# Performance work log

Measured on AMD Instinct MI355X. Metric: run time of the kernel, lower is better.

The kernel has to match this reference:

```python
import jax, jax.numpy as jnp
import numpy as np

N = 100000
E = 1600000
D = 256

def setup_inputs() -> dict:
    key = jax.random.key(0)
    k1, k2, k3 = jax.random.split(key, 3)
    nodes = jax.random.normal(k1, (N, D), dtype=jnp.float32)
    edge_index = jax.random.randint(k2, (2, E), 0, N, dtype=jnp.int64)
    W = jax.random.normal(k3, (D, D), dtype=jnp.float32) * 0.05  # GCN lin weight [out,in]
    b = jnp.zeros((D,), dtype=jnp.float32)
    gamma = jnp.ones((D,), dtype=jnp.float32)
    beta = jnp.zeros((D,), dtype=jnp.float32)
    return {"nodes": nodes, "edge_index": edge_index, "W": W, "b": b,
            "gamma": gamma, "beta": beta}

def reference(nodes, edge_index, W, b, gamma, beta):
    n = nodes.shape[0]
    loop = jnp.arange(n, dtype=edge_index.dtype)
    src = jnp.concatenate([edge_index[0], loop])  # add self-loops (PyG default)
    dst = jnp.concatenate([edge_index[1], loop])
    # linear transform
    x = nodes @ W.T  # [N, D]
    # symmetric normalization: deg from target index, weight 1 per edge
    deg = jnp.zeros((n,), dtype=x.dtype).at[dst].add(1.0)
    dinv = jnp.where(deg > 0, jax.lax.rsqrt(deg), 0.0)
    norm = dinv[src] * dinv[dst]  # [E+N]
    msg = x[src] * norm[:, None]
    out = jax.ops.segment_sum(msg, dst, num_segments=n) + b  # [N, D]
    # LayerNorm over feature dim
    mu = jnp.mean(out, axis=-1, keepdims=True)
    var = jnp.mean(jnp.square(out - mu), axis=-1, keepdims=True)
    out = (out - mu) * jax.lax.rsqrt(var + 1e-5) * gamma + beta
    # ReLU; dropout is identity in eval mode
    return jax.nn.relu(out)
```

## Files before the change

### kernel.cpp

```cpp
#include <hip/hip_runtime.h>
#include <hip/hip_bf16.h>

#define NN 100000
#define EE 1600000
#define DD 256
#define CAP 48
#define NPART 391
#define ABLK 800
#define ACHUNK 2000

typedef __bf16 bf16x8 __attribute__((ext_vector_type(8)));
typedef float f32x4 __attribute__((ext_vector_type(4)));
typedef float f32x2 __attribute__((ext_vector_type(2)));

__device__ __forceinline__ unsigned short f2bf(float f) {
    unsigned u = __builtin_bit_cast(unsigned, f);
    u += 0x7fffu + ((u >> 16) & 1u);
    return (unsigned short)(u >> 16);
}
__device__ __forceinline__ float bf2f(unsigned short h) {
    unsigned u = ((unsigned)h) << 16;
    return __builtin_bit_cast(float, u);
}

__global__ __launch_bounds__(256) void k_partA(const void* __restrict__ eptr,
        unsigned int* __restrict__ gseg2, int* __restrict__ cnts, int* __restrict__ pref) {
    __shared__ int lcnt[NPART];
    __shared__ int lcnt2[NPART];
    __shared__ int lpref[NPART];
    __shared__ int sA[512], sB[512];
    __shared__ __align__(16) unsigned int stash[ACHUNK];
    __shared__ unsigned short stashp[ACHUNK];
    __shared__ __align__(16) unsigned int sorted[ACHUNK];
    __shared__ int lflag;
    const int b = blockIdx.x, tid = threadIdx.x;
    if (tid == 0) lflag = 0;
    for (int i = tid; i < NPART; i += 256) { lcnt[i] = 0; lcnt2[i] = 0; }
    __syncthreads();
    if (tid < 64) {
        const unsigned long long w = ((const unsigned long long*)eptr)[tid];
        if (w > 0xFFFFFFFFULL) lflag = 1;
    }
    __syncthreads();
    const int is32 = lflag;
    const int e0 = b * ACHUNK;
    for (int e = e0 + tid; e < e0 + ACHUNK; e += 256) {
        int ss, dd;
        if (is32) { const int* p = (const int*)eptr; ss = p[e]; dd = p[EE + e]; }
        else { const long long* p = (const long long*)eptr; ss = (int)p[e]; dd = (int)p[EE + e]; }
        const int li = e - e0;
        stash[li]  = ((unsigned)ss << 8) | (unsigned)(dd & 255);
        stashp[li] = (unsigned short)(dd >> 8);
        atomicAdd(&lcnt[dd >> 8], 1);
    }
    __syncthreads();
    sA[tid]       = (tid < NPART) ? lcnt[tid] : 0;
    sA[tid + 256] = (tid + 256 < NPART) ? lcnt[tid + 256] : 0;
    __syncthreads();
    int* s = sA; int* d2 = sB;
    for (int off = 1; off < 512; off <<= 1) {
        d2[tid]       = s[tid]       + (tid >= off ? s[tid - off] : 0);
        d2[tid + 256] = s[tid + 256] + (tid + 256 >= off ? s[tid + 256 - off] : 0);
        __syncthreads();
        int* t = s; s = d2; d2 = t;
    }
    for (int i = tid; i < NPART; i += 256) {
        lpref[i] = (i == 0) ? 0 : s[i - 1];
        cnts[(size_t)i * ABLK + b] = lcnt[i];
        pref[(size_t)i * ABLK + b] = (i == 0) ? 0 : s[i - 1];
    }
    __syncthreads();
    for (int li = tid; li < ACHUNK; li += 256) {
        const unsigned int w = stash[li];
        const int pp = stashp[li];
        const int slot = atomicAdd(&lcnt2[pp], 1);
        sorted[lpref[pp] + slot] = w;
    }
    __syncthreads();
    for (int li4 = tid; li4 < ACHUNK / 4; li4 += 256)
        *(uint4*)(gseg2 + (size_t)b * ACHUNK + (size_t)li4 * 4) = *(const uint4*)&sorted[li4 * 4];
}

__global__ __launch_bounds__(256) void k_partB(const unsigned int* __restrict__ gseg2,
        const int* __restrict__ cnts, const int* __restrict__ pref,
        int* __restrict__ bucket, int* __restrict__ cnt) {
    __shared__ int lc[256];
    __shared__ __align__(16) int lb[256 * CAP];
    const int p = blockIdx.x, tid = threadIdx.x;
    const int node0 = p * 256 + tid;
    lc[tid] = 1;
    lb[tid * CAP] = node0;
    __syncthreads();
    for (int bb = tid; bb < ABLK; bb += 256) {
        const int c = cnts[(size_t)p * ABLK + bb];
        const unsigned int* seg = gseg2 + (size_t)bb * ACHUNK + pref[(size_t)p * ABLK + bb];
        for (int i = 0; i < c; ++i) {
            const unsigned int en = seg[i];
            const int d = en & 255;
            const int slot = atomicAdd(&lc[d], 1);
            if (slot < CAP) lb[d * CAP + slot] = (int)(en >> 8);
        }
    }
    __syncthreads();
    const size_t base = (size_t)p * 256 * CAP;
    #pragma unroll
    for (int it = 0; it < CAP / 4; ++it) {
        const int idx4 = it * 256 + tid;
        const int node = p * 256 + idx4 / (CAP / 4);
        if (node < NN)
            *(uint4*)(bucket + base + (size_t)idx4 * 4) = *(const uint4*)&lb[idx4 * 4];
    }
    if (node0 < NN) cnt[node0] = lc[tid];
}

__global__ void k_detect(const unsigned long long* __restrict__ e64, int* __restrict__ flag) {
    if (threadIdx.x == 0 && blockIdx.x == 0) {
        int is32 = 0;
        for (int i = 0; i < 64; ++i)
            if (e64[i] > 0xFFFFFFFFULL) is32 = 1;
        *flag = is32;
    }
}
__global__ __launch_bounds__(256) void k_init(int* __restrict__ cnt, int* __restrict__ bucket) {
    int v = blockIdx.x * 256 + threadIdx.x;
    if (v < NN) { cnt[v] = 1; bucket[(size_t)v * CAP] = v; }
}
__global__ __launch_bounds__(256) void k_count_scatter(const void* __restrict__ eptr,
        const int* __restrict__ flag, int* __restrict__ cnt, int* __restrict__ bucket) {
    int e = blockIdx.x * 256 + threadIdx.x;
    if (e >= EE) return;
    int s, d;
    if (*flag) { const int* p = (const int*)eptr; s = p[e]; d = p[EE + e]; }
    else { const long long* p = (const long long*)eptr; s = (int)p[e]; d = (int)p[EE + e]; }
    int slot = atomicAdd(&cnt[d], 1);
    if (slot < CAP) bucket[(size_t)d * CAP + slot] = s;
}

__global__ __launch_bounds__(256) void k_wconv(const float* __restrict__ W,
        unsigned short* __restrict__ wf) {
    const int s = blockIdx.x * 256 + threadIdx.x;
    const int lane = s & 63;
    const int ks = (s >> 6) & 7;
    const int g  = (s >> 9) & 3;
    const int wv = s >> 11;
    const int feat = wv * 64 + g * 16 + (lane & 15);
    const int k0 = ks * 32 + (lane >> 4) * 8;
    const float* wp = W + (size_t)feat * 256 + k0;
    unsigned short o[8];
    #pragma unroll
    for (int j = 0; j < 8; ++j) o[j] = f2bf(wp[j]);
    uint4 pk;
    pk.x = o[0] | ((unsigned)o[1] << 16); pk.y = o[2] | ((unsigned)o[3] << 16);
    pk.z = o[4] | ((unsigned)o[5] << 16); pk.w = o[6] | ((unsigned)o[7] << 16);
    *(uint4*)(wf + (size_t)s * 8) = pk;
}

__global__ __launch_bounds__(256) void k_gemm(const float* __restrict__ nodes,
        const unsigned short* __restrict__ wf, const int* __restrict__ cnt,
        unsigned short* __restrict__ y) {
    __shared__ __align__(16) unsigned short xlds[64][264];
    const int tid = threadIdx.x, lane = tid & 63, wv = tid >> 6;
    const int q = lane >> 4, n0 = lane & 15;

    bf16x8 afrag[8][4];
    #pragma unroll
    for (int g = 0; g < 4; ++g)
        #pragma unroll
        for (int ks = 0; ks < 8; ++ks)
            afrag[ks][g] = *(const bf16x8*)(wf + ((((size_t)wv * 4 + g) * 8 + ks) * 64 + lane) * 8);

    const int row0 = blockIdx.x * 64;
    #pragma unroll
    for (int rr = 0; rr < 16; ++rr) {
        const int idx = rr * 256 + tid;
        const int r = idx >> 6, c4 = idx & 63;
        const int grow = min(row0 + r, NN - 1);
        const float4 v = *(const float4*)(nodes + (size_t)grow * 256 + c4 * 4);
        uint2 pk;
        pk.x = (unsigned)f2bf(v.x) | ((unsigned)f2bf(v.y) << 16);
        pk.y = (unsigned)f2bf(v.z) | ((unsigned)f2bf(v.w) << 16);
        *(uint2*)&xlds[r][c4 * 4] = pk;
    }
    __syncthreads();

    #pragma unroll
    for (int sub = 0; sub < 4; ++sub) {
        f32x4 acc[4] = {{0,0,0,0},{0,0,0,0},{0,0,0,0},{0,0,0,0}};
        #pragma unroll
        for (int ks = 0; ks < 8; ++ks) {
            const bf16x8 xf = *(const bf16x8*)&xlds[sub * 16 + n0][ks * 32 + q * 8];
            #pragma unroll
            for (int g = 0; g < 4; ++g)
                acc[g] = __builtin_amdgcn_mfma_f32_16x16x32_bf16(afrag[ks][g], xf, acc[g], 0, 0, 0);
        }
        const int node = row0 + sub * 16 + n0;
        if (node < NN) {
            const float dval = rsqrtf((float)cnt[node]);
            unsigned short* yp = y + (size_t)node * 256 + wv * 64 + q * 4;
            #pragma unroll
            for (int g = 0; g < 4; ++g) {
                uint2 pk;
                pk.x = (unsigned)f2bf(acc[g][0] * dval) | ((unsigned)f2bf(acc[g][1] * dval) << 16);
                pk.y = (unsigned)f2bf(acc[g][2] * dval) | ((unsigned)f2bf(acc[g][3] * dval) << 16);
                *(uint2*)(yp + g * 16) = pk;
            }
        }
    }
}

__global__ __launch_bounds__(256) void k_gather(const unsigned short* __restrict__ y,
        const int* __restrict__ cnt, const int* __restrict__ bucket,
        const float* __restrict__ bias, const float* __restrict__ gamma,
        const float* __restrict__ beta, float* __restrict__ out) {
    const int v = blockIdx.x * 4 + (threadIdx.x >> 6);
    const int lane = threadIdx.x & 63;
    const int h = lane >> 5, l = lane & 31;
    const int c = cnt[v];
    const int m = min(c, CAP);
    const int my = (lane < m) ? bucket[(size_t)v * CAP + lane] : 0;

    f32x2 a2[4] = {{0,0},{0,0},{0,0},{0,0}};
    #define ACCUM(P) do {                                                      \
        a2[0] += (f32x2){__builtin_bit_cast(float, (P).x << 16),               \
                         __builtin_bit_cast(float, (P).x & 0xffff0000u)};      \
        a2[1] += (f32x2){__builtin_bit_cast(float, (P).y << 16),               \
                         __builtin_bit_cast(float, (P).y & 0xffff0000u)};      \
        a2[2] += (f32x2){__builtin_bit_cast(float, (P).z << 16),               \
                         __builtin_bit_cast(float, (P).z & 0xffff0000u)};      \
        a2[3] += (f32x2){__builtin_bit_cast(float, (P).w << 16),               \
                         __builtin_bit_cast(float, (P).w & 0xffff0000u)};      \
    } while (0)

    int j = 0;
    for (; j + 8 <= m; j += 8) {
        const int s0 = __shfl(my, j + h);
        const int s1 = __shfl(my, j + 2 + h);
        const int s2 = __shfl(my, j + 4 + h);
        const int s3 = __shfl(my, j + 6 + h);
        const uint4 p0 = *((const uint4*)(y + (size_t)s0 * 256) + l);
        const uint4 p1 = *((const uint4*)(y + (size_t)s1 * 256) + l);
        const uint4 p2 = *((const uint4*)(y + (size_t)s2 * 256) + l);
        const uint4 p3 = *((const uint4*)(y + (size_t)s3 * 256) + l);
        ACCUM(p0); ACCUM(p1); ACCUM(p2); ACCUM(p3);
    }
    for (; j + 4 <= m; j += 4) {
        const int s0 = __shfl(my, j + h);
        const int s1 = __shfl(my, j + 2 + h);
        const uint4 p0 = *((const uint4*)(y + (size_t)s0 * 256) + l);
        const uint4 p1 = *((const uint4*)(y + (size_t)s1 * 256) + l);
        ACCUM(p0); ACCUM(p1);
    }
    for (; j + 2 <= m; j += 2) {
        const int s0 = __shfl(my, j + h);
        const uint4 p0 = *((const uint4*)(y + (size_t)s0 * 256) + l);
        ACCUM(p0);
    }
    if (j < m) {
        const int st = __shfl(my, j);
        if (h == 0) {
            const uint4 p0 = *((const uint4*)(y + (size_t)st * 256) + l);
            ACCUM(p0);
        }
    }
    #undef ACCUM

    float acc[8];
    acc[0] = a2[0].x; acc[1] = a2[0].y; acc[2] = a2[1].x; acc[3] = a2[1].y;
    acc[4] = a2[2].x; acc[5] = a2[2].y; acc[6] = a2[3].x; acc[7] = a2[3].y;

    #pragma unroll
    for (int i = 0; i < 8; ++i) acc[i] += __shfl_xor(acc[i], 32);

    const float dvv = rsqrtf((float)c);
    const float4 b0 = *(const float4*)(bias + l * 8);
    const float4 b1 = *(const float4*)(bias + l * 8 + 4);
    float u[8];
    u[0] = acc[0] * dvv + b0.x; u[1] = acc[1] * dvv + b0.y;
    u[2] = acc[2] * dvv + b0.z; u[3] = acc[3] * dvv + b0.w;
    u[4] = acc[4] * dvv + b1.x; u[5] = acc[5] * dvv + b1.y;
    u[6] = acc[6] * dvv + b1.z; u[7] = acc[7] * dvv + b1.w;

    float s1 = 0, s2 = 0;
    #pragma unroll
    for (int i = 0; i < 8; ++i) { s1 += u[i]; s2 += u[i] * u[i]; }
    #pragma unroll
    for (int o = 16; o > 0; o >>= 1) {
        s1 += __shfl_xor(s1, o);
        s2 += __shfl_xor(s2, o);
    }
    const float mean = s1 * (1.0f / 256.0f);
    const float var  = s2 * (1.0f / 256.0f) - mean * mean;
    const float rstd = rsqrtf(var + 1e-5f);

    const float4 g0 = *(const float4*)(gamma + l * 8);
    const float4 g1 = *(const float4*)(gamma + l * 8 + 4);
    const float4 e0 = *(const float4*)(beta + l * 8);
    const float4 e1 = *(const float4*)(beta + l * 8 + 4);
    float o8[8];
    o8[0] = fmaxf(0.0f, (u[0] - mean) * rstd * g0.x + e0.x);
    o8[1] = fmaxf(0.0f, (u[1] - mean) * rstd * g0.y + e0.y);
    o8[2] = fmaxf(0.0f, (u[2] - mean) * rstd * g0.z + e0.z);
    o8[3] = fmaxf(0.0f, (u[3] - mean) * rstd * g0.w + e0.w);
    o8[4] = fmaxf(0.0f, (u[4] - mean) * rstd * g1.x + e1.x);
    o8[5] = fmaxf(0.0f, (u[5] - mean) * rstd * g1.y + e1.y);
    o8[6] = fmaxf(0.0f, (u[6] - mean) * rstd * g1.z + e1.z);
    o8[7] = fmaxf(0.0f, (u[7] - mean) * rstd * g1.w + e1.w);
    float4 ov;
    if (h == 0) { ov.x = o8[0]; ov.y = o8[1]; ov.z = o8[2]; ov.w = o8[3]; }
    else        { ov.x = o8[4]; ov.y = o8[5]; ov.z = o8[6]; ov.w = o8[7]; }
    *(float4*)(out + (size_t)v * 256 + l * 8 + h * 4) = ov;
}

extern "C" void kernel_launch(void* const* d_in, const int* in_sizes, int n_in,
                              void* d_out, int out_size, void* d_ws, size_t ws_size,
                              hipStream_t stream) {
    const float* nodes = (const float*)d_in[0];
    const void*  edges = d_in[1];
    const float* W     = (const float*)d_in[2];
    const float* b     = (const float*)d_in[3];
    const float* gamma = (const float*)d_in[4];
    const float* beta  = (const float*)d_in[5];
    float* out = (float*)d_out;

    char* ws = (char*)d_ws;
    size_t off = 0;
    auto alloc = [&](size_t bytes) { size_t p = off; off = (off + bytes + 255) & ~(size_t)255; return p; };
    int*            cnt    = (int*)(ws + alloc((size_t)NN * 4));
    int*            flag   = (int*)(ws + alloc(256));
    int*            bucket = (int*)(ws + alloc((size_t)NN * CAP * 4));
    unsigned short* y      = (unsigned short*)(ws + alloc((size_t)NN * DD * 2));
    unsigned short* wf     = (unsigned short*)(ws + alloc((size_t)DD * DD * 2));
    int*            cnts   = (int*)(ws + alloc((size_t)NPART * ABLK * 4));
    int*            pref   = (int*)(ws + alloc((size_t)NPART * ABLK * 4));
    unsigned int*   gseg2  = (unsigned int*)(ws + alloc((size_t)EE * 4));
    const size_t full_need = off;
    (void)in_sizes; (void)n_in; (void)out_size;

    k_wconv<<<32, 256, 0, stream>>>(W, wf);
    if (ws_size >= full_need) {
        k_partA<<<ABLK, 256, 0, stream>>>(edges, gseg2, cnts, pref);
        k_partB<<<NPART, 256, 0, stream>>>(gseg2, cnts, pref, bucket, cnt);
    } else {
        k_detect<<<1, 64, 0, stream>>>((const unsigned long long*)edges, flag);
        k_init<<<(NN + 255) / 256, 256, 0, stream>>>(cnt, bucket);
        k_count_scatter<<<(EE + 255) / 256, 256, 0, stream>>>(edges, flag, cnt, bucket);
    }
    k_gemm<<<(NN + 63) / 64, 256, 0, stream>>>(nodes, wf, cnt, y);
    k_gather<<<NN / 4, 256, 0, stream>>>(y, cnt, bucket, b, gamma, beta, out);
}
```

Measured before the change: 368.5 us.

## Software-pipeline gather loads, restructure GEMM loop order, use packed bf16 convert

The gather kernel now double-buffers its neighbor-row loads, issuing the next batch of eight rows before accumulating the current batch, so memory latency overlaps with the adds. The bucket index load becomes unconditional, which reads past valid entries when the count is below the lane index (the values are only used up to the count). The GEMM now loads weight fragments per k-step instead of holding all of them in registers, and keeps 16 accumulators across four sub-tiles. Float-to-bf16 conversion switches to the hardware packed convert instruction. These trade register pressure and loop structure for better latency hiding and fewer ALU instructions, and the unconditional bucket read may touch uninitialized slots.

```diff
diff --git a/kernel.cpp b/kernel.cpp
--- a/kernel.cpp
+++ b/kernel.cpp
@@ -21,6 +21,11 @@
 __device__ __forceinline__ float bf2f(unsigned short h) {
     unsigned u = ((unsigned)h) << 16;
     return __builtin_bit_cast(float, u);
+}
+__device__ __forceinline__ unsigned cvtpk(float a, float b) {
+    unsigned r;
+    asm("v_cvt_pk_bf16_f32 %0, %1, %2" : "=v"(r) : "v"(a), "v"(b));
+    return r;
 }
 
 __global__ __launch_bounds__(256) void k_partA(const void* __restrict__ eptr,
@@ -162,13 +167,6 @@
     const int tid = threadIdx.x, lane = tid & 63, wv = tid >> 6;
     const int q = lane >> 4, n0 = lane & 15;
 
-    bf16x8 afrag[8][4];
-    #pragma unroll
-    for (int g = 0; g < 4; ++g)
-        #pragma unroll
-        for (int ks = 0; ks < 8; ++ks)
-            afrag[ks][g] = *(const bf16x8*)(wf + ((((size_t)wv * 4 + g) * 8 + ks) * 64 + lane) * 8);
-
     const int row0 = blockIdx.x * 64;
     #pragma unroll
     for (int rr = 0; rr < 16; ++rr) {
@@ -177,31 +175,46 @@
         const int grow = min(row0 + r, NN - 1);
         const float4 v = *(const float4*)(nodes + (size_t)grow * 256 + c4 * 4);
         uint2 pk;
-        pk.x = (unsigned)f2bf(v.x) | ((unsigned)f2bf(v.y) << 16);
-        pk.y = (unsigned)f2bf(v.z) | ((unsigned)f2bf(v.w) << 16);
+        pk.x = cvtpk(v.x, v.y);
+        pk.y = cvtpk(v.z, v.w);
         *(uint2*)&xlds[r][c4 * 4] = pk;
     }
     __syncthreads();
 
-    #pragma unroll
-    for (int sub = 0; sub < 4; ++sub) {
-        f32x4 acc[4] = {{0,0,0,0},{0,0,0,0},{0,0,0,0},{0,0,0,0}};
+    f32x4 acc[4][4];
+    #pragma unroll
+    for (int sub = 0; sub < 4; ++sub)
         #pragma unroll
-        for (int ks = 0; ks < 8; ++ks) {
+        for (int g = 0; g < 4; ++g) acc[sub][g] = (f32x4){0, 0, 0, 0};
+
+    #pragma unroll
+    for (int ks = 0; ks < 8; ++ks) {
+        bf16x8 a[4];
+        #pragma unroll
+        for (int g = 0; g < 4; ++g)
+            a[g] = *(const bf16x8*)(wf + ((((size_t)wv * 4 + g) * 8 + ks) * 64 + lane) * 8);
+        #pragma unroll
+        for (int sub = 0; sub < 4; ++sub) {
             const bf16x8 xf = *(const bf16x8*)&xlds[sub * 16 + n0][ks * 32 + q * 8];
             #pragma unroll
             for (int g = 0; g < 4; ++g)
-                acc[g] = __builtin_amdgcn_mfma_f32_16x16x32_bf16(afrag[ks][g], xf, acc[g], 0, 0, 0);
+                acc[sub][g] = __builtin_amdgcn_mfma_f32_16x16x32_bf16(a[g], xf, acc[sub][g], 0, 0, 0);
         }
+    }
+
+    #pragma unroll
+    for (int sub = 0; sub < 4; ++sub) {
         const int node = row0 + sub * 16 + n0;
         if (node < NN) {
             const float dval = rsqrtf((float)cnt[node]);
             unsigned short* yp = y + (size_t)node * 256 + wv * 64 + q * 4;
             #pragma unroll
             for (int g = 0; g < 4; ++g) {
+                const float e0 = acc[sub][g][0] * dval, e1 = acc[sub][g][1] * dval;
+                const float e2 = acc[sub][g][2] * dval, e3 = acc[sub][g][3] * dval;
                 uint2 pk;
-                pk.x = (unsigned)f2bf(acc[g][0] * dval) | ((unsigned)f2bf(acc[g][1] * dval) << 16);
-                pk.y = (unsigned)f2bf(acc[g][2] * dval) | ((unsigned)f2bf(acc[g][3] * dval) << 16);
+                pk.x = cvtpk(e0, e1);
+                pk.y = cvtpk(e2, e3);
                 *(uint2*)(yp + g * 16) = pk;
             }
         }
@@ -216,8 +229,8 @@
     const int lane = threadIdx.x & 63;
     const int h = lane >> 5, l = lane & 31;
     const int c = cnt[v];
+    const int my = bucket[(size_t)v * CAP + lane];
     const int m = min(c, CAP);
-    const int my = (lane < m) ? bucket[(size_t)v * CAP + lane] : 0;
 
     f32x2 a2[4] = {{0,0},{0,0},{0,0},{0,0}};
     #define ACCUM(P) do {                                                      \
@@ -232,16 +245,29 @@
     } while (0)
 
     int j = 0;
-    for (; j + 8 <= m; j += 8) {
-        const int s0 = __shfl(my, j + h);
-        const int s1 = __shfl(my, j + 2 + h);
-        const int s2 = __shfl(my, j + 4 + h);
-        const int s3 = __shfl(my, j + 6 + h);
-        const uint4 p0 = *((const uint4*)(y + (size_t)s0 * 256) + l);
-        const uint4 p1 = *((const uint4*)(y + (size_t)s1 * 256) + l);
-        const uint4 p2 = *((const uint4*)(y + (size_t)s2 * 256) + l);
-        const uint4 p3 = *((const uint4*)(y + (size_t)s3 * 256) + l);
-        ACCUM(p0); ACCUM(p1); ACCUM(p2); ACCUM(p3);
+    uint4 P0 = {0,0,0,0}, P1 = {0,0,0,0}, P2 = {0,0,0,0}, P3 = {0,0,0,0};
+    const bool have8 = (m >= 8);
+    if (have8) {
+        const int s0 = __shfl(my, 0 + h), s1 = __shfl(my, 2 + h);
+        const int s2 = __shfl(my, 4 + h), s3 = __shfl(my, 6 + h);
+        P0 = *((const uint4*)(y + (size_t)s0 * 256) + l);
+        P1 = *((const uint4*)(y + (size_t)s1 * 256) + l);
+        P2 = *((const uint4*)(y + (size_t)s2 * 256) + l);
+        P3 = *((const uint4*)(y + (size_t)s3 * 256) + l);
+    }
+    for (; j + 16 <= m; j += 8) {
+        const int s0 = __shfl(my, j + 8 + h),  s1 = __shfl(my, j + 10 + h);
+        const int s2 = __shfl(my, j + 12 + h), s3 = __shfl(my, j + 14 + h);
+        const uint4 q0 = *((const uint4*)(y + (size_t)s0 * 256) + l);
+        const uint4 q1 = *((const uint4*)(y + (size_t)s1 * 256) + l);
+        const uint4 q2 = *((const uint4*)(y + (size_t)s2 * 256) + l);
+        const uint4 q3 = *((const uint4*)(y + (size_t)s3 * 256) + l);
+        ACCUM(P0); ACCUM(P1); ACCUM(P2); ACCUM(P3);
+        P0 = q0; P1 = q1; P2 = q2; P3 = q3;
+    }
+    if (have8) {
+        ACCUM(P0); ACCUM(P1); ACCUM(P2); ACCUM(P3);
+        j += 8;
     }
     for (; j + 4 <= m; j += 4) {
         const int s0 = __shfl(my, j + h);
```

After: 374.7 us. No clear change (+1.7%).
